# Optimization experiments

Measured on AMD Instinct MI355X. Metric: run time of the kernel, lower is better.

Reference implementation:

```python
import jax, jax.numpy as jnp
import numpy as np

N = 100_000   # nodes
E = 1_600_000 # edges
C = 64        # in = hidden = out channels
H = 8         # heads
D = C // H    # head_dim = 8
R = 4         # relations
L = 2         # layers


def setup_inputs() -> dict:
    key = jax.random.key(0)
    ks = jax.random.split(key, 10)
    sc = 1.0 / np.sqrt(C)  # xavier-ish scale
    return {
        "x": jax.random.normal(ks[0], (N, C), jnp.float32),
        "edge_index": jax.random.randint(ks[1], (2, E), 0, N),
        "edge_type": jax.random.randint(ks[2], (E,), 0, R),
        "W_Q": jax.random.normal(ks[3], (L, R, H, C, D), jnp.float32) * sc,
        "W_K": jax.random.normal(ks[4], (L, R, H, C, D), jnp.float32) * sc,
        "W_V": jax.random.normal(ks[5], (L, R, H, C, D), jnp.float32) * sc,
        "W_concat": jax.random.normal(ks[6], (L, R, H * D, C), jnp.float32) * sc,
        "sem_w": jax.random.normal(ks[7], (L, C), jnp.float32) * sc,
        "sem_b": jnp.zeros((L,), jnp.float32),
        "W_self": jax.random.normal(ks[8], (L, C, C), jnp.float32) * sc,
        "ln_g": jnp.ones((L, C), jnp.float32),
        "ln_b": jnp.zeros((L, C), jnp.float32),
    }


def _layer(x, src, dst, edge_type, WQ, WK, WV, Wcat, sw, sb, Ws, g, b):
    inv_sqrt_d = 1.0 / np.sqrt(D)
    rel_msgs = []
    for r in range(R):  # small fixed relation loop
        mask = (edge_type == r).astype(x.dtype)             # (E,)
        Q = jnp.einsum('nc,hcd->nhd', x, WQ[r])             # (N,H,D)
        K = jnp.einsum('nc,hcd->nhd', x, WK[r])
        V = jnp.einsum('nc,hcd->nhd', x, WV[r])
        # edge-wise QK energy, leaky_relu(0.01), scatter-add into dst node
        energy = jnp.einsum('ehd,ehd->eh', Q[dst], K[src]) * inv_sqrt_d
        energy = jax.nn.leaky_relu(energy)                  # (E,H)
        alpha_n = jax.ops.segment_sum(energy * mask[:, None], dst,
                                      num_segments=N)       # (N,H)
        alpha = jax.nn.softmax(alpha_n, axis=0)             # softmax over nodes
        w = alpha[dst] * mask[:, None]                      # (E,H)
        m = jax.ops.segment_sum(w[:, :, None] * V[src], dst,
                                num_segments=N)             # (N,H,D)
        rel_msgs.append(m.reshape(N, H * D) @ Wcat[r])      # (N,C)
    stacked = jnp.stack(rel_msgs)                           # (R,N,C)
    beta = jax.nn.softmax(stacked @ sw + sb, axis=0)        # (R,N) semantic attn
    agg = jnp.einsum('rn,rnc->nc', beta, stacked)           # (N,C)
    y = x + jax.nn.gelu(x @ Ws + agg, approximate=False)
    mu = y.mean(-1, keepdims=True)
    var = y.var(-1, keepdims=True)
    return (y - mu) / jnp.sqrt(var + 1e-5) * g + b


def reference(x, edge_index, edge_type, W_Q, W_K, W_V, W_concat,
              sem_w, sem_b, W_self, ln_g, ln_b):
    src, dst = edge_index[0], edge_index[1]  # PyG source_to_target: j=row0, i=row1
    for l in range(L):
        x = _layer(x, src, dst, edge_type, W_Q[l], W_K[l], W_V[l], W_concat[l],
                   sem_w[l], sem_b[l], W_self[l], ln_g[l], ln_b[l])
        # inter-layer dropout omitted (inference / eval mode)
    return x
```

## Files before the change

kernel.cpp:

```cpp
#include <hip/hip_runtime.h>
#include <hip/hip_bf16.h>

#define NN 100000
#define EE 1600000
#define RRR 4
#define HHH 8
#define NT 400000
#define GG 782
#define SHIFT 9
#define NBLK 512
#define CHUNK 3125
#define BMAX 2560

typedef unsigned int u32;
typedef unsigned short u16;
typedef __attribute__((ext_vector_type(8))) short bf16x8;
typedef __attribute__((ext_vector_type(4))) float f32x4;

static constexpr size_t OFF_KV   = 0;
static constexpr size_t OFF_Q    = 25600000;
static constexpr size_t OFF_S    = 76800000;
static constexpr size_t OFF_AL   = 128000000;
static constexpr size_t OFF_PW   = 140800000;
static constexpr size_t OFF_PART = 141100000;
static constexpr size_t OFF_FIN  = 141110000;
static constexpr size_t OFF_ROWP = 141365504;
static constexpr size_t OFF_EDG  = 142965512;
static constexpr size_t OFF_BSTORE = OFF_S;
static constexpr size_t OFF_HIST   = OFF_S + 8000000;
static constexpr size_t OFF_OFFA   = OFF_S + 16000000;
static constexpr size_t OFF_BASE   = OFF_S + 24000000;

__device__ inline u16 f2bf(float f){
  union { __hip_bfloat16 h; u16 u; } cv; cv.h = __float2bfloat16(f); return cv.u;
}
__device__ inline float bf2f(u16 u){ return __uint_as_float(((u32)u) << 16); }

__global__ __launch_bounds__(256) void k_histA(const int* __restrict__ dst, const int* __restrict__ typ,
                                               u32* __restrict__ Hist){
  __shared__ u32 h[GG];
  int b = blockIdx.x, t = threadIdx.x;
  for (int g = t; g < GG; g += 256) h[g] = 0u;
  __syncthreads();
  int e0 = b * CHUNK;
  for (int e = e0 + t; e < e0 + CHUNK; e += 256){
    int seg = typ[e] * NN + dst[e];
    atomicAdd(&h[seg >> SHIFT], 1u);
  }
  __syncthreads();
  for (int g = t; g < GG; g += 256) Hist[(size_t)b * GG + g] = h[g];
}

__global__ __launch_bounds__(1024) void k_base(const u32* __restrict__ Hist, u32* __restrict__ Base,
                                               u32* __restrict__ rowp){
  __shared__ u32 tot[GG];
  int t = threadIdx.x;
  if (t < GG){
    u32 s = 0;
    for (int b = 0; b < NBLK; b++) s += Hist[(size_t)b * GG + t];
    tot[t] = s;
  }
  __syncthreads();
  if (t == 0){
    u32 acc = 0;
    for (int g = 0; g < GG; g++){ u32 c = tot[g]; Base[g] = acc; acc += c; }
    Base[GG] = acc;
    rowp[NT] = EE;
  }
}

__global__ __launch_bounds__(512) void k_off(const u32* __restrict__ Hist, const u32* __restrict__ Base,
                                             u32* __restrict__ Off){
  __shared__ u32 v[NBLK];
  int g = blockIdx.x, t = threadIdx.x;
  v[t] = Hist[(size_t)t * GG + g];
  __syncthreads();
  if (t == 0){
    u32 acc = Base[g];
    for (int b = 0; b < NBLK; b++){ u32 c = v[b]; v[b] = acc; acc += c; }
  }
  __syncthreads();
  Off[(size_t)g * NBLK + t] = v[t];
}

__global__ __launch_bounds__(256) void k_fill(const int* __restrict__ src, const int* __restrict__ dst,
                                              const int* __restrict__ typ, const u32* __restrict__ Off,
                                              u32* __restrict__ bstore){
  __shared__ u32 cur[GG];
  int b = blockIdx.x, t = threadIdx.x;
  for (int g = t; g < GG; g += 256) cur[g] = Off[(size_t)g * NBLK + b];
  __syncthreads();
  int e0 = b * CHUNK;
  for (int e = e0 + t; e < e0 + CHUNK; e += 256){
    int seg = typ[e] * NN + dst[e];
    u32 pos = atomicAdd(&cur[seg >> SHIFT], 1u);
    bstore[pos] = ((u32)(seg & 511) << 17) | (u32)src[e];
  }
}

__global__ __launch_bounds__(256) void k_sortD(const u32* __restrict__ bstore, const u32* __restrict__ Base,
                                               u32* __restrict__ rowp, u32* __restrict__ edges){
  __shared__ u32 ent[BMAX];
  __shared__ u32 binc[512], bexc[512];
  int g = blockIdx.x, t = threadIdx.x;
  u32 base = Base[g];
  u32 cnt = Base[g + 1] - base;
  if (cnt > (u32)BMAX) cnt = (u32)BMAX;
  for (int i = t; i < 512; i += 256) binc[i] = 0u;
  __syncthreads();
  for (u32 i = t; i < cnt; i += 256){
    u32 v = bstore[base + i];
    ent[i] = v;
    atomicAdd(&binc[v >> 17], 1u);
  }
  __syncthreads();
  if (t == 0){
    u32 acc = 0;
    #pragma unroll 8
    for (int s = 0; s < 512; s++){ u32 c = binc[s]; bexc[s] = acc; binc[s] = acc; acc += c; }
  }
  __syncthreads();
  for (int s = t; s < 512; s += 256){
    int seg = g * 512 + s;
    if (seg < NT) rowp[seg] = base + bexc[s];
  }
  __syncthreads();
  for (u32 i = t; i < cnt; i += 256){
    u32 v = ent[i];
    u32 p = atomicAdd(&binc[v >> 17], 1u);
    edges[base + p] = v & 0x1FFFFu;
  }
}

__global__ __launch_bounds__(256) void k_repackbf(const float* __restrict__ WQ, const float* __restrict__ WK,
                                                  const float* __restrict__ WV, const float* __restrict__ Wcat,
                                                  const float* __restrict__ Wself, u16* __restrict__ pwB){
  int t = blockIdx.x * 256 + threadIdx.x;
  if (t >= 2 * 17 * 4096) return;
  int l = t / (17 * 4096), rem = t % (17 * 4096);
  int mat = rem >> 12, idx = rem & 4095;
  int out = idx >> 6, c = idx & 63;
  float v;
  if (mat < 12){
    int kind = mat >> 2, r = mat & 3;
    int h = out >> 3, d = out & 7;
    const float* Wsrc = (kind == 0) ? WQ : (kind == 1) ? WK : WV;
    v = Wsrc[((((l * RRR + r) * HHH + h) * 64) + c) * 8 + d];
  } else if (mat == 12){
    v = Wself[(l * 64 + c) * 64 + out];
  } else {
    int r = mat - 13;
    v = Wcat[(((l * RRR + r) * 64) + c) * 64 + out];
  }
  pwB[t] = f2bf(v);
}


__global__ __launch_bounds__(256) void k_qkv(const float* __restrict__ x,
                                             const u16* __restrict__ pwQ, const u16* __restrict__ pwK,
                                             const u16* __restrict__ pwV,
                                             u16* __restrict__ Qr, u32* __restrict__ kvp){
  __shared__ u16 xa[64][72];
  __shared__ u16 wt[3][64][72];
  int t = threadIdx.x;
  int n0 = blockIdx.x * 64;
  {
    int row = t >> 2, c0 = (t & 3) * 16;
    int n = n0 + row;
    float4 v0 = {}, v1 = {}, v2 = {}, v3 = {};
    if (n < NN){
      const float4* xp = (const float4*)(x + (size_t)n * 64 + c0);
      v0 = xp[0]; v1 = xp[1]; v2 = xp[2]; v3 = xp[3];
    }
    ushort4* dp = (ushort4*)&xa[row][c0];
    dp[0] = make_ushort4(f2bf(v0.x), f2bf(v0.y), f2bf(v0.z), f2bf(v0.w));
    dp[1] = make_ushort4(f2bf(v1.x), f2bf(v1.y), f2bf(v1.z), f2bf(v1.w));
    dp[2] = make_ushort4(f2bf(v2.x), f2bf(v2.y), f2bf(v2.z), f2bf(v2.w));
    dp[3] = make_ushort4(f2bf(v3.x), f2bf(v3.y), f2bf(v3.z), f2bf(v3.w));
  }
  {
    const u32* p0 = (const u32*)pwQ;
    const u32* p1 = (const u32*)pwK;
    const u32* p2 = (const u32*)pwV;
    for (int idx = t; idx < 3 * 2048; idx += 256){
      int m = idx >> 11, rem = idx & 2047;
      int out = rem >> 5, cc = rem & 31;
      u32 w = (m == 0) ? p0[rem] : (m == 1) ? p1[rem] : p2[rem];
      *(u32*)&wt[m][out][cc * 2] = w;
    }
  }
  __syncthreads();
  int w = t >> 6, lane = t & 63;
  int ra = w * 16 + (lane & 15);
  int kg = (lane >> 4) * 8;
  int cb = lane & 15;
  int rb = (lane >> 4) * 4;
  bf16x8 a0 = *(const bf16x8*)&xa[ra][kg];
  bf16x8 a1 = *(const bf16x8*)&xa[ra][32 + kg];
  f32x4 z = {0.f, 0.f, 0.f, 0.f};
  {
    f32x4 acc[4] = {z, z, z, z};
    #pragma unroll
    for (int t4 = 0; t4 < 4; t4++){
      bf16x8 b0 = *(const bf16x8*)&wt[0][t4 * 16 + cb][kg];
      bf16x8 b1 = *(const bf16x8*)&wt[0][t4 * 16 + cb][32 + kg];
      acc[t4] = __builtin_amdgcn_mfma_f32_16x16x32_bf16(a0, b0, acc[t4], 0, 0, 0);
      acc[t4] = __builtin_amdgcn_mfma_f32_16x16x32_bf16(a1, b1, acc[t4], 0, 0, 0);
    }
    #pragma unroll
    for (int t4 = 0; t4 < 4; t4++){
      #pragma unroll
      for (int i = 0; i < 4; i++){
        int n = n0 + w * 16 + rb + i;
        if (n < NN) Qr[(size_t)n * 64 + t4 * 16 + cb] = f2bf(acc[t4][i]);
      }
    }
  }
  {
    f32x4 ak[4] = {z, z, z, z};
    f32x4 av[4] = {z, z, z, z};
    #pragma unroll
    for (int t4 = 0; t4 < 4; t4++){
      bf16x8 bk0 = *(const bf16x8*)&wt[1][t4 * 16 + cb][kg];
      bf16x8 bk1 = *(const bf16x8*)&wt[1][t4 * 16 + cb][32 + kg];
      bf16x8 bv0 = *(const bf16x8*)&wt[2][t4 * 16 + cb][kg];
      bf16x8 bv1 = *(const bf16x8*)&wt[2][t4 * 16 + cb][32 + kg];
      ak[t4] = __builtin_amdgcn_mfma_f32_16x16x32_bf16(a0, bk0, ak[t4], 0, 0, 0);
      ak[t4] = __builtin_amdgcn_mfma_f32_16x16x32_bf16(a1, bk1, ak[t4], 0, 0, 0);
      av[t4] = __builtin_amdgcn_mfma_f32_16x16x32_bf16(a0, bv0, av[t4], 0, 0, 0);
      av[t4] = __builtin_amdgcn_mfma_f32_16x16x32_bf16(a1, bv1, av[t4], 0, 0, 0);
    }
    #pragma unroll
    for (int t4 = 0; t4 < 4; t4++){
      #pragma unroll
      for (int i = 0; i < 4; i++){
        int n = n0 + w * 16 + rb + i;
        if (n < NN) kvp[(size_t)n * 64 + t4 * 16 + cb] = (u32)f2bf(ak[t4][i]) | ((u32)f2bf(av[t4][i]) << 16);
      }
    }
  }
}

__global__ __launch_bounds__(256) void k_self(const float* __restrict__ x, const u16* __restrict__ pwS,
                                              u16* __restrict__ outb){
  __shared__ u16 xa[64][72];
  __shared__ u16 wt[64][72];
  int t = threadIdx.x;
  int n0 = blockIdx.x * 64;
  {
    int row = t >> 2, c0 = (t & 3) * 16;
    int n = n0 + row;
    float4 v0 = {}, v1 = {}, v2 = {}, v3 = {};
    if (n < NN){
      const float4* xp = (const float4*)(x + (size_t)n * 64 + c0);
      v0 = xp[0]; v1 = xp[1]; v2 = xp[2]; v3 = xp[3];
    }
    ushort4* dp = (ushort4*)&xa[row][c0];
    dp[0] = make_ushort4(f2bf(v0.x), f2bf(v0.y), f2bf(v0.z), f2bf(v0.w));
    dp[1] = make_ushort4(f2bf(v1.x), f2bf(v1.y), f2bf(v1.z), f2bf(v1.w));
    dp[2] = make_ushort4(f2bf(v2.x), f2bf(v2.y), f2bf(v2.z), f2bf(v2.w));
    dp[3] = make_ushort4(f2bf(v3.x), f2bf(v3.y), f2bf(v3.z), f2bf(v3.w));
  }
  {
    const u32* p0 = (const u32*)pwS;
    for (int idx = t; idx < 2048; idx += 256){
      int out = idx >> 5, cc = idx & 31;
      *(u32*)&wt[out][cc * 2] = p0[idx];
    }
  }
  __syncthreads();
  int w = t >> 6, lane = t & 63;
  int ra = w * 16 + (lane & 15);
  int kg = (lane >> 4) * 8;
  int cb = lane & 15;
  int rb = (lane >> 4) * 4;
  bf16x8 a0 = *(const bf16x8*)&xa[ra][kg];
  bf16x8 a1 = *(const bf16x8*)&xa[ra][32 + kg];
  f32x4 z = {0.f, 0.f, 0.f, 0.f};
  f32x4 acc[4] = {z, z, z, z};
  #pragma unroll
  for (int t4 = 0; t4 < 4; t4++){
    bf16x8 b0 = *(const bf16x8*)&wt[t4 * 16 + cb][kg];
    bf16x8 b1 = *(const bf16x8*)&wt[t4 * 16 + cb][32 + kg];
    acc[t4] = __builtin_amdgcn_mfma_f32_16x16x32_bf16(a0, b0, acc[t4], 0, 0, 0);
    acc[t4] = __builtin_amdgcn_mfma_f32_16x16x32_bf16(a1, b1, acc[t4], 0, 0, 0);
  }
  #pragma unroll
  for (int t4 = 0; t4 < 4; t4++){
    #pragma unroll
    for (int i = 0; i < 4; i++){
      int n = n0 + w * 16 + rb + i;
      if (n < NN) outb[(size_t)n * 64 + t4 * 16 + cb] = f2bf(acc[t4][i]);
    }
  }
}

__global__ __launch_bounds__(256) void k_gather(const u32* __restrict__ edges, const u32* __restrict__ rowpR,
                                                const u32* __restrict__ kvp, const u16* __restrict__ Qr,
                                                u16* __restrict__ Sr, float* __restrict__ alphaR){
  int wid = threadIdx.x >> 6, lane = threadIdx.x & 63;
  int n = blockIdx.x * 4 + wid;
  float q = bf2f(Qr[(size_t)n * 64 + lane]);
  u32 beg = rowpR[n], end = rowpR[n + 1];
  float sa = 0.f, aa = 0.f;
  const float inv_sqrt_d = 0.35355339059327373f;
  for (u32 base = beg; base < end; base += 64){
    u32 cnt = (end - base < 64u) ? (end - base) : 64u;
    u32 eidx = (base + (u32)lane < end) ? edges[base + lane] : 0u;
    u32 j = 0;
    for (; j + 4 <= cnt; j += 4){
      int s0 = __shfl((int)eidx, (int)j);
      int s1 = __shfl((int)eidx, (int)j + 1);
      int s2 = __shfl((int)eidx, (int)j + 2);
      int s3 = __shfl((int)eidx, (int)j + 3);
      u32 w0 = kvp[(size_t)s0 * 64 + lane];
      u32 w1 = kvp[(size_t)s1 * 64 + lane];
      u32 w2 = kvp[(size_t)s2 * 64 + lane];
      u32 w3 = kvp[(size_t)s3 * 64 + lane];
      float p0 = q * bf2f((u16)(w0 & 0xFFFFu));
      float p1 = q * bf2f((u16)(w1 & 0xFFFFu));
      float p2 = q * bf2f((u16)(w2 & 0xFFFFu));
      float p3 = q * bf2f((u16)(w3 & 0xFFFFu));
      p0 += __shfl_xor(p0, 1); p1 += __shfl_xor(p1, 1); p2 += __shfl_xor(p2, 1); p3 += __shfl_xor(p3, 1);
      p0 += __shfl_xor(p0, 2); p1 += __shfl_xor(p1, 2); p2 += __shfl_xor(p2, 2); p3 += __shfl_xor(p3, 2);
      p0 += __shfl_xor(p0, 4); p1 += __shfl_xor(p1, 4); p2 += __shfl_xor(p2, 4); p3 += __shfl_xor(p3, 4);
      float e0 = p0 * inv_sqrt_d; e0 = (e0 > 0.f) ? e0 : 0.01f * e0;
      float e1 = p1 * inv_sqrt_d; e1 = (e1 > 0.f) ? e1 : 0.01f * e1;
      float e2 = p2 * inv_sqrt_d; e2 = (e2 > 0.f) ? e2 : 0.01f * e2;
      float e3 = p3 * inv_sqrt_d; e3 = (e3 > 0.f) ? e3 : 0.01f * e3;
      aa += (e0 + e1) + (e2 + e3);
      sa += (bf2f((u16)(w0 >> 16)) + bf2f((u16)(w1 >> 16))) +
            (bf2f((u16)(w2 >> 16)) + bf2f((u16)(w3 >> 16)));
    }
    for (; j < cnt; ++j){
      int s = __shfl((int)eidx, (int)j);
      u32 w = kvp[(size_t)s * 64 + lane];
      float p = q * bf2f((u16)(w & 0xFFFFu));
      p += __shfl_xor(p, 1);
      p += __shfl_xor(p, 2);
      p += __shfl_xor(p, 4);
      float e = p * inv_sqrt_d;
      e = (e > 0.f) ? e : 0.01f * e;
      aa += e;
      sa += bf2f((u16)(w >> 16));
    }
  }
  Sr[(size_t)n * 64 + lane] = f2bf(sa);
  if ((lane & 7) == 0) alphaR[(size_t)n * 8 + (lane >> 3)] = aa;
}

__global__ __launch_bounds__(256) void k_stats1(const float* __restrict__ alpha, float2* __restrict__ part){
  int col = blockIdx.x;
  int r = col >> 3, h = col & 7;
  int chunk = blockIdx.y;
  const int per = (NN + 31) / 32;
  int nbeg = chunk * per;
  int nend = nbeg + per; if (nend > NN) nend = NN;
  int t = threadIdx.x;
  float m = -1e30f, s = 0.f;
  for (int n = nbeg + t; n < nend; n += 256){
    float a = alpha[((size_t)r * NN + n) * 8 + h];
    if (a > m){ s *= expf(m - a); m = a; }
    s += expf(a - m);
  }
  __shared__ float sm[256], ss[256];
  sm[t] = m; ss[t] = s; __syncthreads();
  for (int off = 128; off > 0; off >>= 1){
    if (t < off){
      float m2 = sm[t + off], s2 = ss[t + off];
      float M = fmaxf(sm[t], m2);
      ss[t] = ss[t] * expf(sm[t] - M) + s2 * expf(m2 - M);
      sm[t] = M;
    }
    __syncthreads();
  }
  if (t == 0) part[col * 32 + chunk] = make_float2(sm[0], ss[0]);
}

__global__ void k_stats2(const float2* __restrict__ part, float2* __restrict__ fin){
  int col = threadIdx.x;
  if (col < 32){
    float M = -1e30f, S = 0.f;
    for (int i = 0; i < 32; i++){
      float2 p = part[col * 32 + i];
      float Mn = fmaxf(M, p.x);
      S = S * expf(M - Mn) + p.y * expf(p.x - Mn);
      M = Mn;
    }
    fin[col] = make_float2(M, 1.f / S);
  }
}

__global__ __launch_bounds__(256) void k_msg(const u16* __restrict__ S, const float* __restrict__ alpha,
                                             const float2* __restrict__ fin, const u16* __restrict__ pwCat,
                                             u16* __restrict__ stacked){
  __shared__ u16 xa[64][72];
  __shared__ u16 wt[64][72];
  int r = blockIdx.y;
  int t = threadIdx.x;
  int n0 = blockIdx.x * 64;
  {
    int row = t >> 2, c0 = (t & 3) * 16;
    int n = n0 + row;
    int na = (n < NN) ? n : (NN - 1);
    int h0 = c0 >> 3;
    float2 f0 = fin[r * 8 + h0];
    float2 f1 = fin[r * 8 + h0 + 1];
    float a0 = alpha[((size_t)r * NN + na) * 8 + h0];
    float a1 = alpha[((size_t)r * NN + na) * 8 + h0 + 1];
    float w0 = expf(a0 - f0.x) * f0.y;
    float w1 = expf(a1 - f1.x) * f1.y;
    const u32* sp = (const u32*)(S + ((size_t)r * NN + na) * 64 + c0);
    #pragma unroll
    for (int jj = 0; jj < 8; jj++){
      u32 bts = sp[jj];
      float wm = (jj < 4) ? w0 : w1;
      ushort2 o;
      o.x = f2bf(bf2f((u16)(bts & 0xFFFFu)) * wm);
      o.y = f2bf(bf2f((u16)(bts >> 16)) * wm);
      *(ushort2*)&xa[row][c0 + jj * 2] = o;
    }
  }
  {
    const u32* p0 = (const u32*)(pwCat + (size_t)r * 4096);
    for (int idx = t; idx < 2048; idx += 256){
      int out = idx >> 5, cc = idx & 31;
      *(u32*)&wt[out][cc * 2] = p0[idx];
    }
  }
  __syncthreads();
  int w = t >> 6, lane = t & 63;
  int ra = w * 16 + (lane & 15);
  int kg = (lane >> 4) * 8;
  int cb = lane & 15;
  int rb = (lane >> 4) * 4;
  bf16x8 a0 = *(const bf16x8*)&xa[ra][kg];
  bf16x8 a1 = *(const bf16x8*)&xa[ra][32 + kg];
  f32x4 z = {0.f, 0.f, 0.f, 0.f};
  f32x4 acc[4] = {z, z, z, z};
  #pragma unroll
  for (int t4 = 0; t4 < 4; t4++){
    bf16x8 b0 = *(const bf16x8*)&wt[t4 * 16 + cb][kg];
    bf16x8 b1 = *(const bf16x8*)&wt[t4 * 16 + cb][32 + kg];
    acc[t4] = __builtin_amdgcn_mfma_f32_16x16x32_bf16(a0, b0, acc[t4], 0, 0, 0);
    acc[t4] = __builtin_amdgcn_mfma_f32_16x16x32_bf16(a1, b1, acc[t4], 0, 0, 0);
  }
  #pragma unroll
  for (int t4 = 0; t4 < 4; t4++){
    #pragma unroll
    for (int i = 0; i < 4; i++){
      int n = n0 + w * 16 + rb + i;
      if (n < NN) stacked[((size_t)r * NN + n) * 64 + t4 * 16 + cb] = f2bf(acc[t4][i]);
    }
  }
}

__global__ __launch_bounds__(256) void k_final(const u16* __restrict__ stacked, const u16* __restrict__ selfb,
                                               const float* __restrict__ xin,
                                               const float* __restrict__ semw, const float* __restrict__ semb,
                                               const float* __restrict__ lng, const float* __restrict__ lnb,
                                               float* __restrict__ xout){
  int t = threadIdx.x;
  int wid = t >> 6, lane = t & 63;
  int n = blockIdx.x * 4 + wid;
  float st[4];
  #pragma unroll
  for (int r = 0; r < 4; r++) st[r] = bf2f(stacked[((size_t)r * NN + n) * 64 + lane]);
  float sw = semw[lane];
  float lg[4];
  #pragma unroll
  for (int r = 0; r < 4; r++){
    float p = st[r] * sw;
    #pragma unroll
    for (int o = 1; o < 64; o <<= 1) p += __shfl_xor(p, o);
    lg[r] = p + semb[0];
  }
  float mx = fmaxf(fmaxf(lg[0], lg[1]), fmaxf(lg[2], lg[3]));
  float e0 = expf(lg[0] - mx), e1 = expf(lg[1] - mx), e2 = expf(lg[2] - mx), e3 = expf(lg[3] - mx);
  float inv = 1.f / (e0 + e1 + e2 + e3);
  float agg = (e0 * st[0] + e1 * st[1] + e2 * st[2] + e3 * st[3]) * inv;
  float pre = bf2f(selfb[(size_t)n * 64 + lane]) + agg;
  float ge = 0.5f * pre * (1.f + erff(pre * 0.70710678118654752f));
  float y = xin[(size_t)n * 64 + lane] + ge;
  float mu = y;
  #pragma unroll
  for (int o = 1; o < 64; o <<= 1) mu += __shfl_xor(mu, o);
  mu *= (1.f / 64.f);
  float d = y - mu;
  float vv = d * d;
  #pragma unroll
  for (int o = 1; o < 64; o <<= 1) vv += __shfl_xor(vv, o);
  vv *= (1.f / 64.f);
  xout[(size_t)n * 64 + lane] = d * rsqrtf(vv + 1e-5f) * lng[lane] + lnb[lane];
}

extern "C" void kernel_launch(void* const* d_in, const int* in_sizes, int n_in,
                              void* d_out, int out_size, void* d_ws, size_t ws_size,
                              hipStream_t stream){
  const float* x0    = (const float*)d_in[0];
  const int*   eidx  = (const int*)d_in[1];
  const int*   etyp  = (const int*)d_in[2];
  const float* WQ    = (const float*)d_in[3];
  const float* WK    = (const float*)d_in[4];
  const float* WV    = (const float*)d_in[5];
  const float* Wcat  = (const float*)d_in[6];
  const float* semw  = (const float*)d_in[7];
  const float* semb  = (const float*)d_in[8];
  const float* Wself = (const float*)d_in[9];
  const float* lng   = (const float*)d_in[10];
  const float* lnb   = (const float*)d_in[11];
  float* out = (float*)d_out;
  char* ws = (char*)d_ws;

  const int* srcArr = eidx;
  const int* dstArr = eidx + EE;

  u32*  kvp      = (u32*)(ws + OFF_KV);
  u16*  selfb    = (u16*)(ws + OFF_KV);
  u16*  Qb       = (u16*)(ws + OFF_Q);
  u16*  stackedB = (u16*)(ws + OFF_Q);
  u16*  Sb       = (u16*)(ws + OFF_S);
  float* alphaB  = (float*)(ws + OFF_AL);
  u16*  pwB      = (u16*)(ws + OFF_PW);
  float2* part   = (float2*)(ws + OFF_PART);
  float2* fin    = (float2*)(ws + OFF_FIN);
  u32* rowp   = (u32*)(ws + OFF_ROWP);
  u32* edges  = (u32*)(ws + OFF_EDG);
  u32* bstore = (u32*)(ws + OFF_BSTORE);
  u32* Hist   = (u32*)(ws + OFF_HIST);
  u32* Off    = (u32*)(ws + OFF_OFFA);
  u32* Base   = (u32*)(ws + OFF_BASE);

  k_histA<<<NBLK, 256, 0, stream>>>(dstArr, etyp, Hist);
  k_base<<<1, 1024, 0, stream>>>(Hist, Base, rowp);
  k_off<<<GG, 512, 0, stream>>>(Hist, Base, Off);
  k_fill<<<NBLK, 256, 0, stream>>>(srcArr, dstArr, etyp, Off, bstore);
  k_sortD<<<GG, 256, 0, stream>>>(bstore, Base, rowp, edges);
  k_repackbf<<<(2 * 17 * 4096 + 255) / 256, 256, 0, stream>>>(WQ, WK, WV, Wcat, Wself, pwB);

  for (int l = 0; l < 2; l++){
    const float* xcur = (l == 0) ? x0 : out;
    const u16* pwL = pwB + (size_t)l * 17 * 4096;
    for (int r = 0; r < 4; r++){
      k_qkv<<<1563, 256, 0, stream>>>(xcur, pwL + (size_t)r * 4096, pwL + (size_t)(4 + r) * 4096,
                                      pwL + (size_t)(8 + r) * 4096, Qb + (size_t)r * NN * 64, kvp);
      k_gather<<<NN / 4, 256, 0, stream>>>(edges, rowp + (size_t)r * NN, kvp,
                                           Qb + (size_t)r * NN * 64,
                                           Sb + (size_t)r * NN * 64,
                                           alphaB + (size_t)r * NN * 8);
    }
    k_self<<<1563, 256, 0, stream>>>(xcur, pwL + (size_t)12 * 4096, selfb);
    k_stats1<<<dim3(32, 32), 256, 0, stream>>>(alphaB, part);
    k_stats2<<<1, 64, 0, stream>>>(part, fin);
    k_msg<<<dim3(1563, 4), 256, 0, stream>>>(Sb, alphaB, fin, pwL + (size_t)13 * 4096, stackedB);
    k_final<<<NN / 4, 256, 0, stream>>>(stackedB, selfb, xcur,
                                        semw + l * 64, semb + l, lng + l * 64, lnb + l * 64, out);
  }
  (void)in_sizes; (void)n_in; (void)out_size; (void)ws_size;
}
```

Baseline: 710.7 us.

## Split gather wave into half-waves and precompute semantic logits in message kernel

The edge gather kernel now has each half of the wavefront handle a different edge. Each lane loads two K/V pairs with a 64-bit load, so every loop iteration covers twice as many edges, with one fewer shuffle-reduction step and a cross-half combine at the end. The semantic attention logits are folded algebraically: Wcat·sem_w is precomputed once and the logit is accumulated in k_msg, which removes four full-wave reductions per node in k_final. semb is dropped because it cancels in the softmax. k_stats1 is reorganised so each block reads all 8 heads contiguously, which makes the alpha reads coalesced.

```diff
diff --git a/kernel.cpp b/kernel.cpp
--- a/kernel.cpp
+++ b/kernel.cpp
@@ -24,8 +24,10 @@
 static constexpr size_t OFF_PW   = 140800000;
 static constexpr size_t OFF_PART = 141100000;
 static constexpr size_t OFF_FIN  = 141110000;
+static constexpr size_t OFF_CW   = 141120000;
 static constexpr size_t OFF_ROWP = 141365504;
 static constexpr size_t OFF_EDG  = 142965512;
+static constexpr size_t OFF_LG   = 149400000;
 static constexpr size_t OFF_BSTORE = OFF_S;
 static constexpr size_t OFF_HIST   = OFF_S + 8000000;
 static constexpr size_t OFF_OFFA   = OFF_S + 16000000;
@@ -155,6 +157,18 @@
   pwB[t] = f2bf(v);
 }
 
+__global__ __launch_bounds__(512) void k_cw(const float* __restrict__ Wcat, const float* __restrict__ semw,
+                                            float* __restrict__ cw){
+  int t = threadIdx.x;
+  int l = t >> 8, r = (t >> 6) & 3, k = t & 63;
+  const float* wp = Wcat + (((size_t)(l * RRR + r) * 64) + k) * 64;
+  const float* sp = semw + l * 64;
+  float s = 0.f;
+  #pragma unroll 8
+  for (int c = 0; c < 64; c++) s += wp[c] * sp[c];
+  cw[t] = s;
+}
+
 
 __global__ __launch_bounds__(256) void k_qkv(const float* __restrict__ x,
                                              const u16* __restrict__ pwQ, const u16* __restrict__ pwK,
@@ -299,73 +313,87 @@
                                                 const u32* __restrict__ kvp, const u16* __restrict__ Qr,
                                                 u16* __restrict__ Sr, float* __restrict__ alphaR){
   int wid = threadIdx.x >> 6, lane = threadIdx.x & 63;
+  int half = lane >> 5;
+  int i = lane & 31;
   int n = blockIdx.x * 4 + wid;
-  float q = bf2f(Qr[(size_t)n * 64 + lane]);
+  u32 qp = *(const u32*)&Qr[(size_t)n * 64 + 2 * i];
+  float q0 = bf2f((u16)(qp & 0xFFFFu));
+  float q1 = bf2f((u16)(qp >> 16));
   u32 beg = rowpR[n], end = rowpR[n + 1];
-  float sa = 0.f, aa = 0.f;
-  const float inv_sqrt_d = 0.35355339059327373f;
+  float sa0 = 0.f, sa1 = 0.f, aa = 0.f;
+  const float isd = 0.35355339059327373f;
   for (u32 base = beg; base < end; base += 64){
     u32 cnt = (end - base < 64u) ? (end - base) : 64u;
     u32 eidx = (base + (u32)lane < end) ? edges[base + lane] : 0u;
     u32 j = 0;
-    for (; j + 4 <= cnt; j += 4){
-      int s0 = __shfl((int)eidx, (int)j);
-      int s1 = __shfl((int)eidx, (int)j + 1);
-      int s2 = __shfl((int)eidx, (int)j + 2);
-      int s3 = __shfl((int)eidx, (int)j + 3);
-      u32 w0 = kvp[(size_t)s0 * 64 + lane];
-      u32 w1 = kvp[(size_t)s1 * 64 + lane];
-      u32 w2 = kvp[(size_t)s2 * 64 + lane];
-      u32 w3 = kvp[(size_t)s3 * 64 + lane];
-      float p0 = q * bf2f((u16)(w0 & 0xFFFFu));
-      float p1 = q * bf2f((u16)(w1 & 0xFFFFu));
-      float p2 = q * bf2f((u16)(w2 & 0xFFFFu));
-      float p3 = q * bf2f((u16)(w3 & 0xFFFFu));
+    for (; j + 8 <= cnt; j += 8){
+      int s0 = __shfl((int)eidx, (int)(j + half));
+      int s1 = __shfl((int)eidx, (int)(j + 2 + half));
+      int s2 = __shfl((int)eidx, (int)(j + 4 + half));
+      int s3 = __shfl((int)eidx, (int)(j + 6 + half));
+      uint2 w0 = *(const uint2*)&kvp[(size_t)s0 * 64 + 2 * i];
+      uint2 w1 = *(const uint2*)&kvp[(size_t)s1 * 64 + 2 * i];
+      uint2 w2 = *(const uint2*)&kvp[(size_t)s2 * 64 + 2 * i];
+      uint2 w3 = *(const uint2*)&kvp[(size_t)s3 * 64 + 2 * i];
+      float p0 = q0 * bf2f((u16)(w0.x & 0xFFFFu)) + q1 * bf2f((u16)(w0.y & 0xFFFFu));
+      float p1 = q0 * bf2f((u16)(w1.x & 0xFFFFu)) + q1 * bf2f((u16)(w1.y & 0xFFFFu));
+      float p2 = q0 * bf2f((u16)(w2.x & 0xFFFFu)) + q1 * bf2f((u16)(w2.y & 0xFFFFu));
+      float p3 = q0 * bf2f((u16)(w3.x & 0xFFFFu)) + q1 * bf2f((u16)(w3.y & 0xFFFFu));
       p0 += __shfl_xor(p0, 1); p1 += __shfl_xor(p1, 1); p2 += __shfl_xor(p2, 1); p3 += __shfl_xor(p3, 1);
       p0 += __shfl_xor(p0, 2); p1 += __shfl_xor(p1, 2); p2 += __shfl_xor(p2, 2); p3 += __shfl_xor(p3, 2);
-      p0 += __shfl_xor(p0, 4); p1 += __shfl_xor(p1, 4); p2 += __shfl_xor(p2, 4); p3 += __shfl_xor(p3, 4);
-      float e0 = p0 * inv_sqrt_d; e0 = (e0 > 0.f) ? e0 : 0.01f * e0;
-      float e1 = p1 * inv_sqrt_d; e1 = (e1 > 0.f) ? e1 : 0.01f * e1;
-      float e2 = p2 * inv_sqrt_d; e2 = (e2 > 0.f) ? e2 : 0.01f * e2;
-      float e3 = p3 * inv_sqrt_d; e3 = (e3 > 0.f) ? e3 : 0.01f * e3;
+      float e0 = p0 * isd; e0 = (e0 > 0.f) ? e0 : 0.01f * e0;
+      float e1 = p1 * isd; e1 = (e1 > 0.f) ? e1 : 0.01f * e1;
+      float e2 = p2 * isd; e2 = (e2 > 0.f) ? e2 : 0.01f * e2;
+      float e3 = p3 * isd; e3 = (e3 > 0.f) ? e3 : 0.01f * e3;
       aa += (e0 + e1) + (e2 + e3);
-      sa += (bf2f((u16)(w0 >> 16)) + bf2f((u16)(w1 >> 16))) +
-            (bf2f((u16)(w2 >> 16)) + bf2f((u16)(w3 >> 16)));
-    }
-    for (; j < cnt; ++j){
-      int s = __shfl((int)eidx, (int)j);
-      u32 w = kvp[(size_t)s * 64 + lane];
-      float p = q * bf2f((u16)(w & 0xFFFFu));
+      sa0 += (bf2f((u16)(w0.x >> 16)) + bf2f((u16)(w1.x >> 16))) +
+             (bf2f((u16)(w2.x >> 16)) + bf2f((u16)(w3.x >> 16)));
+      sa1 += (bf2f((u16)(w0.y >> 16)) + bf2f((u16)(w1.y >> 16))) +
+             (bf2f((u16)(w2.y >> 16)) + bf2f((u16)(w3.y >> 16)));
+    }
+    for (; j < cnt; j += 2){
+      u32 jj = j + (u32)half;
+      float mk = (jj < cnt) ? 1.f : 0.f;
+      u32 js = (jj < cnt) ? jj : (cnt - 1);
+      int s = __shfl((int)eidx, (int)js);
+      uint2 w = *(const uint2*)&kvp[(size_t)s * 64 + 2 * i];
+      float p = q0 * bf2f((u16)(w.x & 0xFFFFu)) + q1 * bf2f((u16)(w.y & 0xFFFFu));
       p += __shfl_xor(p, 1);
       p += __shfl_xor(p, 2);
-      p += __shfl_xor(p, 4);
-      float e = p * inv_sqrt_d;
-      e = (e > 0.f) ? e : 0.01f * e;
-      aa += e;
-      sa += bf2f((u16)(w >> 16));
-    }
-  }
-  Sr[(size_t)n * 64 + lane] = f2bf(sa);
-  if ((lane & 7) == 0) alphaR[(size_t)n * 8 + (lane >> 3)] = aa;
+      float e = p * isd; e = (e > 0.f) ? e : 0.01f * e;
+      aa += e * mk;
+      sa0 += bf2f((u16)(w.x >> 16)) * mk;
+      sa1 += bf2f((u16)(w.y >> 16)) * mk;
+    }
+  }
+  sa0 += __shfl_xor(sa0, 32);
+  sa1 += __shfl_xor(sa1, 32);
+  aa  += __shfl_xor(aa, 32);
+  if (half == 0){
+    ushort2 o; o.x = f2bf(sa0); o.y = f2bf(sa1);
+    *(ushort2*)&Sr[(size_t)n * 64 + 2 * i] = o;
+    if ((i & 3) == 0) alphaR[(size_t)n * 8 + (i >> 2)] = aa;
+  }
 }
 
 __global__ __launch_bounds__(256) void k_stats1(const float* __restrict__ alpha, float2* __restrict__ part){
-  int col = blockIdx.x;
-  int r = col >> 3, h = col & 7;
-  int chunk = blockIdx.y;
+  int r = blockIdx.y;
+  int chunk = blockIdx.x;
   const int per = (NN + 31) / 32;
   int nbeg = chunk * per;
   int nend = nbeg + per; if (nend > NN) nend = NN;
   int t = threadIdx.x;
+  int h = t & 7;
+  int g = t >> 3;
   float m = -1e30f, s = 0.f;
-  for (int n = nbeg + t; n < nend; n += 256){
+  for (int n = nbeg + g; n < nend; n += 32){
     float a = alpha[((size_t)r * NN + n) * 8 + h];
     if (a > m){ s *= expf(m - a); m = a; }
     s += expf(a - m);
   }
   __shared__ float sm[256], ss[256];
   sm[t] = m; ss[t] = s; __syncthreads();
-  for (int off = 128; off > 0; off >>= 1){
+  for (int off = 128; off >= 8; off >>= 1){
     if (t < off){
       float m2 = sm[t + off], s2 = ss[t + off];
       float M = fmaxf(sm[t], m2);
@@ -374,7 +402,7 @@
     }
     __syncthreads();
   }
-  if (t == 0) part[col * 32 + chunk] = make_float2(sm[0], ss[0]);
+  if (t < 8) part[(r * 8 + t) * 32 + chunk] = make_float2(sm[t], ss[t]);
 }
 
 __global__ void k_stats2(const float2* __restrict__ part, float2* __restrict__ fin){
@@ -393,6 +421,7 @@
 
 __global__ __launch_bounds__(256) void k_msg(const u16* __restrict__ S, const float* __restrict__ alpha,
                                              const float2* __restrict__ fin, const u16* __restrict__ pwCat,
+                                             const float* __restrict__ cwL, float* __restrict__ lgbuf,
                                              u16* __restrict__ stacked){
   __shared__ u16 xa[64][72];
   __shared__ u16 wt[64][72];
@@ -411,15 +440,23 @@
     float w0 = expf(a0 - f0.x) * f0.y;
     float w1 = expf(a1 - f1.x) * f1.y;
     const u32* sp = (const u32*)(S + ((size_t)r * NN + na) * 64 + c0);
+    const float* cwr = cwL + r * 64;
+    float lgp = 0.f;
     #pragma unroll
     for (int jj = 0; jj < 8; jj++){
       u32 bts = sp[jj];
       float wm = (jj < 4) ? w0 : w1;
+      float mv0 = bf2f((u16)(bts & 0xFFFFu)) * wm;
+      float mv1 = bf2f((u16)(bts >> 16)) * wm;
+      lgp += mv0 * cwr[c0 + jj * 2] + mv1 * cwr[c0 + jj * 2 + 1];
       ushort2 o;
-      o.x = f2bf(bf2f((u16)(bts & 0xFFFFu)) * wm);
-      o.y = f2bf(bf2f((u16)(bts >> 16)) * wm);
+      o.x = f2bf(mv0);
+      o.y = f2bf(mv1);
       *(ushort2*)&xa[row][c0 + jj * 2] = o;
     }
+    lgp += __shfl_xor(lgp, 1);
+    lgp += __shfl_xor(lgp, 2);
+    if ((t & 3) == 0 && n < NN) lgbuf[(size_t)r * NN + n] = lgp;
   }
   {
     const u32* p0 = (const u32*)(pwCat + (size_t)r * 4096);
@@ -456,8 +493,7 @@
 }
 
 __global__ __launch_bounds__(256) void k_final(const u16* __restrict__ stacked, const u16* __restrict__ selfb,
-                                               const float* __restrict__ xin,
-                                               const float* __restrict__ semw, const float* __restrict__ semb,
+                                               const float* __restrict__ xin, const float* __restrict__ lgbuf,
                                                const float* __restrict__ lng, const float* __restrict__ lnb,
                                                float* __restrict__ xout){
   int t = threadIdx.x;
@@ -466,17 +502,12 @@
   float st[4];
   #pragma unroll
   for (int r = 0; r < 4; r++) st[r] = bf2f(stacked[((size_t)r * NN + n) * 64 + lane]);
-  float sw = semw[lane];
-  float lg[4];
-  #pragma unroll
-  for (int r = 0; r < 4; r++){
-    float p = st[r] * sw;
-    #pragma unroll
-    for (int o = 1; o < 64; o <<= 1) p += __shfl_xor(p, o);
-    lg[r] = p + semb[0];
-  }
-  float mx = fmaxf(fmaxf(lg[0], lg[1]), fmaxf(lg[2], lg[3]));
-  float e0 = expf(lg[0] - mx), e1 = expf(lg[1] - mx), e2 = expf(lg[2] - mx), e3 = expf(lg[3] - mx);
+  float lg0 = lgbuf[n];
+  float lg1 = lgbuf[(size_t)NN + n];
+  float lg2 = lgbuf[(size_t)2 * NN + n];
+  float lg3 = lgbuf[(size_t)3 * NN + n];
+  float mx = fmaxf(fmaxf(lg0, lg1), fmaxf(lg2, lg3));
+  float e0 = expf(lg0 - mx), e1 = expf(lg1 - mx), e2 = expf(lg2 - mx), e3 = expf(lg3 - mx);
   float inv = 1.f / (e0 + e1 + e2 + e3);
   float agg = (e0 * st[0] + e1 * st[1] + e2 * st[2] + e3 * st[3]) * inv;
   float pre = bf2f(selfb[(size_t)n * 64 + lane]) + agg;
@@ -524,6 +555,8 @@
   u16*  pwB      = (u16*)(ws + OFF_PW);
   float2* part   = (float2*)(ws + OFF_PART);
   float2* fin    = (float2*)(ws + OFF_FIN);
+  float* cw      = (float*)(ws + OFF_CW);
+  float* lgbuf   = (float*)(ws + OFF_LG);
   u32* rowp   = (u32*)(ws + OFF_ROWP);
   u32* edges  = (u32*)(ws + OFF_EDG);
   u32* bstore = (u32*)(ws + OFF_BSTORE);
@@ -537,6 +570,7 @@
   k_fill<<<NBLK, 256, 0, stream>>>(srcArr, dstArr, etyp, Off, bstore);
   k_sortD<<<GG, 256, 0, stream>>>(bstore, Base, rowp, edges);
   k_repackbf<<<(2 * 17 * 4096 + 255) / 256, 256, 0, stream>>>(WQ, WK, WV, Wcat, Wself, pwB);
+  k_cw<<<1, 512, 0, stream>>>(Wcat, semw, cw);
 
   for (int l = 0; l < 2; l++){
     const float* xcur = (l == 0) ? x0 : out;
@@ -550,11 +584,13 @@
                                            alphaB + (size_t)r * NN * 8);
     }
     k_self<<<1563, 256, 0, stream>>>(xcur, pwL + (size_t)12 * 4096, selfb);
-    k_stats1<<<dim3(32, 32), 256, 0, stream>>>(alphaB, part);
+    k_stats1<<<dim3(32, 4), 256, 0, stream>>>(alphaB, part);
     k_stats2<<<1, 64, 0, stream>>>(part, fin);
-    k_msg<<<dim3(1563, 4), 256, 0, stream>>>(Sb, alphaB, fin, pwL + (size_t)13 * 4096, stackedB);
-    k_final<<<NN / 4, 256, 0, stream>>>(stackedB, selfb, xcur,
-                                        semw + l * 64, semb + l, lng + l * 64, lnb + l * 64, out);
+    k_msg<<<dim3(1563, 4), 256, 0, stream>>>(Sb, alphaB, fin, pwL + (size_t)13 * 4096,
+                                             cw + l * 256, lgbuf, stackedB);
+    k_final<<<NN / 4, 256, 0, stream>>>(stackedB, selfb, xcur, lgbuf,
+                                        lng + l * 64, lnb + l * 64, out);
   }
   (void)in_sizes; (void)n_in; (void)out_size; (void)ws_size;
-}
+  (void)semb;
+}
```

Measured after the change: 726.7 us. 1.02x slower.
